# Optimization experiments

Hardware: AMD Instinct MI355X
Metric: run time of the kernel (lower is better)

Reference implementation:

```python
import jax, jax.numpy as jnp
import numpy as np

BITS = 4
MAXQ = 15          # (1 << BITS) - 1
PACK = 32 // BITS  # 8 values packed per int32


def dequantize(qweight, qzeros, scales, g_idx):
    """GPTQ 4-bit dequant. qweight: [K//8, N] int32, qzeros: [G, N//8] int32,
    scales: [G, N] float, g_idx: [K] int32 -> dense W [K, N] float."""
    N = qweight.shape[1]
    shifts = (jnp.arange(PACK, dtype=jnp.uint32) * BITS)  # [8]
    qw = qweight.astype(jnp.uint32)
    # unpack along K: k = row*8 + j  (matches shifter = (k % 8) * bits)
    w_int = ((qw[:, None, :] >> shifts[None, :, None]) & MAXQ).reshape(-1, N)  # [K, N]
    qz = qzeros.astype(jnp.uint32)
    # unpack along N: n = col*8 + j  (matches zeros_shifter = (n % 8) * bits)
    z_int = ((qz[:, :, None] >> shifts[None, None, :]) & MAXQ).reshape(qzeros.shape[0], -1) + 1  # [G, N]
    dt = scales.dtype
    # group-wise dequant: w = (q - zero) * scale, gathered per-row via g_idx
    return (w_int.astype(dt) - z_int[g_idx].astype(dt)) * scales[g_idx]


def setup_inputs() -> dict:
    key = jax.random.key(0)
    k1, k2, k3, k4, k5 = jax.random.split(key, 5)
    M, K, N, GS = 128, 4096, 11008, 128
    G = K // GS
    x = jax.random.normal(k1, (M, K), dtype=jnp.float32)
    qweight = jax.random.randint(k2, (K // PACK, N), 0, 2147483647, dtype=jnp.int32)
    qzeros = jax.random.randint(k3, (G, N // PACK), 0, 2147483647, dtype=jnp.int32)
    scales = jax.random.uniform(k4, (G, N), dtype=jnp.float32, minval=0.001, maxval=0.01)
    bias = jax.random.normal(k5, (N,), dtype=jnp.float32)
    g_idx = (jnp.arange(K, dtype=jnp.int32) // GS).astype(jnp.int32)
    return {"x": x, "qweight": qweight, "qzeros": qzeros, "scales": scales,
            "bias": bias, "g_idx": g_idx}


def reference(x, qweight, qzeros, scales, bias, g_idx):
    w = dequantize(qweight, qzeros, scales, g_idx)  # [K, N]
    return x @ w + bias
```

## Files before the change

### kernel.cpp

```cpp
#include <hip/hip_runtime.h>
#include <stdint.h>


#define M_DIM 128
#define K_DIM 4096
#define N_DIM 11008
#define GS    128
#define SPLIT 4
#define STEPS 32
#define PART_STRIDE ((size_t)M_DIM * N_DIM)

typedef _Float16 half8  __attribute__((ext_vector_type(8)));
typedef _Float16 half4t __attribute__((ext_vector_type(4)));
typedef _Float16 half2t __attribute__((ext_vector_type(2)));
typedef float    f32x4  __attribute__((ext_vector_type(4)));

__global__ void k_prep(const float* __restrict__ x, const int* __restrict__ qzeros,
                       const float* __restrict__ scales,
                       _Float16* __restrict__ xf, half2t* __restrict__ zsc) {
    int b = blockIdx.x, t = threadIdx.x;
    if (b < 256) {
        int slot = b * 256 + t;
        int lane = slot & 63;
        int pair = slot >> 6;
        int mt = pair >> 7, kb = pair & 127;
        int row = mt * 16 + (lane & 15);
        int col = kb * 32 + (lane >> 4) * 8;
        const float* px = x + (size_t)row * K_DIM + col;
        float4 v0 = *(const float4*)px;
        float4 v1 = *(const float4*)(px + 4);
        half8 o;
        o[0] = (_Float16)v0.x; o[1] = (_Float16)v0.y;
        o[2] = (_Float16)v0.z; o[3] = (_Float16)v0.w;
        o[4] = (_Float16)v1.x; o[5] = (_Float16)v1.y;
        o[6] = (_Float16)v1.z; o[7] = (_Float16)v1.w;
        *(half8*)(xf + (size_t)slot * 8) = o;
    } else {
        b -= 256;
        int g = b / 43;
        int n = (b - g * 43) * 256 + t;
        unsigned qz = (unsigned)qzeros[g * (N_DIM / 8) + (n >> 3)];
        float z1 = (float)((qz >> ((n & 7) * 4)) & 15u) + 1.0f;
        float s  = scales[g * N_DIM + n];
        half2t o;
        o[0] = (_Float16)s;
        o[1] = (_Float16)(-z1 * s);
        zsc[g * N_DIM + n] = o;
    }
}

__device__ __forceinline__ half8 dequant8(unsigned q, half2t S2, half2t Z2) {
    const half2t BIAS = __builtin_bit_cast(half2t, 0x64006400u);
    half2t w[4];
#pragma unroll
    for (int p = 0; p < 4; ++p) {
        unsigned r = __builtin_amdgcn_perm(q, q, 0x00010001u * (unsigned)p);
        unsigned t = (r & 0x00F0000Fu) | 0x64006400u;
        w[p] = __builtin_elementwise_fma(__builtin_bit_cast(half2t, t) - BIAS, S2, Z2);
    }
    half4t w01 = __builtin_shufflevector(w[0], w[1], 0, 1, 2, 3);
    half4t w23 = __builtin_shufflevector(w[2], w[3], 0, 1, 2, 3);
    return __builtin_shufflevector(w01, w23, 0, 1, 2, 3, 4, 5, 6, 7);
}

__global__ __launch_bounds__(256, 4)
void k_gemm(const _Float16* __restrict__ xf,
            const int*      __restrict__ qweight,
            const half2t*   __restrict__ zsc,
            float*          __restrict__ part)
{
    const int tid  = threadIdx.x;
    const int lane = tid & 63;
    const int w    = tid >> 6;
    const int q    = lane >> 4;
    const int lr   = lane & 15;

    const int n0 = blockIdx.x * 64;
    const int by = blockIdx.y;

    int ncol[4];
#pragma unroll
    for (int j = 0; j < 4; ++j) ncol[j] = n0 + j * 16 + lr;

    f32x4 acc[2][4];
#pragma unroll
    for (int f = 0; f < 2; ++f)
#pragma unroll
        for (int j = 0; j < 4; ++j)
            acc[f][j] = (f32x4){0.f, 0.f, 0.f, 0.f};

    const _Float16* pa0 = xf + (((size_t)(2 * w) * 128 + by * 32) << 9) + lane * 8;
    const _Float16* pa1 = pa0 + ((size_t)128 << 9);
    const int* pq = qweight + (size_t)(by * 128 + q) * N_DIM;
    const half2t* pz = zsc + (size_t)(by * 8) * N_DIM;

    half8 a0 = *(const half8*)pa0;
    half8 a1 = *(const half8*)pa1;
    unsigned qc[4];
    half2t   zc[4];
#pragma unroll
    for (int j = 0; j < 4; ++j) {
        qc[j] = (unsigned)pq[ncol[j]];
        zc[j] = pz[ncol[j]];
    }

    for (int g = 0; g < 8; ++g) {
        const half2t SC = { (_Float16)1.0f, (_Float16)0.0625f };
        half2t S2[4], Z2[4];
#pragma unroll
        for (int j = 0; j < 4; ++j) {
            half2t ss = __builtin_shufflevector(zc[j], zc[j], 0, 0);
            S2[j] = ss * SC;
            Z2[j] = __builtin_shufflevector(zc[j], zc[j], 1, 1);
        }

#pragma unroll
        for (int t = 0; t < 4; ++t) {
            const int s  = g * 4 + t;
            const int sn = (s + 1 < STEPS) ? s + 1 : s;

            half8 na0 = *(const half8*)(pa0 + (size_t)sn * 512);
            half8 na1 = *(const half8*)(pa1 + (size_t)sn * 512);
            unsigned nq[4];
#pragma unroll
            for (int j = 0; j < 4; ++j)
                nq[j] = (unsigned)pq[(size_t)sn * 4 * N_DIM + ncol[j]];
            half2t nz[4];
            if (t == 3) {
                int gn = (g + 1 < 8) ? g + 1 : g;
#pragma unroll
                for (int j = 0; j < 4; ++j)
                    nz[j] = pz[(size_t)gn * N_DIM + ncol[j]];
            }

#pragma unroll
            for (int j = 0; j < 4; ++j) {
                half8 bf = dequant8(qc[j], S2[j], Z2[j]);
                acc[0][j] = __builtin_amdgcn_mfma_f32_16x16x32_f16(a0, bf, acc[0][j], 0, 0, 0);
                acc[1][j] = __builtin_amdgcn_mfma_f32_16x16x32_f16(a1, bf, acc[1][j], 0, 0, 0);
            }

            a0 = na0; a1 = na1;
#pragma unroll
            for (int j = 0; j < 4; ++j) qc[j] = nq[j];
            if (t == 3) {
#pragma unroll
                for (int j = 0; j < 4; ++j) zc[j] = nz[j];
            }
        }
    }

    float* po = part + (size_t)by * PART_STRIDE;
#pragma unroll
    for (int f = 0; f < 2; ++f) {
        int mrow = w * 32 + f * 16 + q * 4;
#pragma unroll
        for (int j = 0; j < 4; ++j)
#pragma unroll
            for (int r = 0; r < 4; ++r)
                po[(size_t)(mrow + r) * N_DIM + ncol[j]] = acc[f][j][r];
    }
}

__global__ void k_reduce(const float* __restrict__ part, const float* __restrict__ bias,
                         float* __restrict__ out) {
    int i = (blockIdx.x * 256 + threadIdx.x) * 4;
    int m = i / N_DIM;
    int n = i - m * N_DIM;
    f32x4 s = *(const f32x4*)(bias + n);
#pragma unroll
    for (int sp = 0; sp < SPLIT; ++sp)
        s += *(const f32x4*)(part + sp * PART_STRIDE + i);
    *(f32x4*)(out + i) = s;
}

extern "C" void kernel_launch(void* const* d_in, const int* in_sizes, int n_in,
                              void* d_out, int out_size, void* d_ws, size_t ws_size,
                              hipStream_t stream) {
    const float* x       = (const float*)d_in[0];
    const int*   qweight = (const int*)d_in[1];
    const int*   qzeros  = (const int*)d_in[2];
    const float* scales  = (const float*)d_in[3];
    const float* bias    = (const float*)d_in[4];

    char* ws = (char*)d_ws;
    _Float16* xf   = (_Float16*)ws;
    half2t*   zsc  = (half2t*)(ws + 1048576);
    float*    part = (float*)(ws + 1048576 + 1409024);

    k_prep  <<<dim3(1632),            dim3(256), 0, stream>>>(x, qzeros, scales, xf, zsc);
    k_gemm  <<<dim3(N_DIM/64, SPLIT), dim3(256), 0, stream>>>(xf, qweight, zsc, part);
    k_reduce<<<dim3(1376),            dim3(256), 0, stream>>>(part, bias, (float*)d_out);
}
```

Measured before the change: 110.3 us.

## Remove split-K and reduce kernel; write output with bias directly from GEMM

Drops the 4-way split-K and its partial-sum buffer and reduce kernel. Each of the 172 blocks now runs all 128 K-steps and adds the bias in its epilogue. It also deepens the register prefetch of activations and weights to two steps ahead. This avoids writing and re-reading four fp32 partial outputs (about 22 MB) and one launch, but cuts the grid to 172 blocks on a 256-CU device, so parallelism drops and fewer loads are in flight.

```diff
diff --git a/kernel.cpp b/kernel.cpp
--- a/kernel.cpp
+++ b/kernel.cpp
@@ -6,9 +6,7 @@
 #define K_DIM 4096
 #define N_DIM 11008
 #define GS    128
-#define SPLIT 4
-#define STEPS 32
-#define PART_STRIDE ((size_t)M_DIM * N_DIM)
+#define STEPS 128
 
 typedef _Float16 half8  __attribute__((ext_vector_type(8)));
 typedef _Float16 half4t __attribute__((ext_vector_type(4)));
@@ -67,7 +65,8 @@
 void k_gemm(const _Float16* __restrict__ xf,
             const int*      __restrict__ qweight,
             const half2t*   __restrict__ zsc,
-            float*          __restrict__ part)
+            const float*    __restrict__ bias,
+            float*          __restrict__ out)
 {
     const int tid  = threadIdx.x;
     const int lane = tid & 63;
@@ -76,7 +75,6 @@
     const int lr   = lane & 15;
 
     const int n0 = blockIdx.x * 64;
-    const int by = blockIdx.y;
 
     int ncol[4];
 #pragma unroll
@@ -89,22 +87,29 @@
         for (int j = 0; j < 4; ++j)
             acc[f][j] = (f32x4){0.f, 0.f, 0.f, 0.f};
 
-    const _Float16* pa0 = xf + (((size_t)(2 * w) * 128 + by * 32) << 9) + lane * 8;
+    const _Float16* pa0 = xf + (((size_t)(2 * w) * 128) << 9) + lane * 8;
     const _Float16* pa1 = pa0 + ((size_t)128 << 9);
-    const int* pq = qweight + (size_t)(by * 128 + q) * N_DIM;
-    const half2t* pz = zsc + (size_t)(by * 8) * N_DIM;
+    const int*      pq  = qweight + (size_t)q * N_DIM;
+    const half2t*   pz  = zsc;
 
-    half8 a0 = *(const half8*)pa0;
-    half8 a1 = *(const half8*)pa1;
-    unsigned qc[4];
+    half8    A0[2], A1[2];
+    unsigned Q[2][4];
     half2t   zc[4];
 #pragma unroll
-    for (int j = 0; j < 4; ++j) {
-        qc[j] = (unsigned)pq[ncol[j]];
-        zc[j] = pz[ncol[j]];
+    for (int c = 0; c < 2; ++c) {
+        A0[c] = *(const half8*)(pa0 + (size_t)c * 512);
+        A1[c] = *(const half8*)(pa1 + (size_t)c * 512);
+#pragma unroll
+        for (int j = 0; j < 4; ++j)
+            Q[c][j] = (unsigned)pq[(size_t)c * 4 * N_DIM + ncol[j]];
     }
+#pragma unroll
+    for (int j = 0; j < 4; ++j) zc[j] = pz[ncol[j]];
+    float bv[4];
+#pragma unroll
+    for (int j = 0; j < 4; ++j) bv[j] = bias[ncol[j]];
 
-    for (int g = 0; g < 8; ++g) {
+    for (int g = 0; g < 32; ++g) {
         const half2t SC = { (_Float16)1.0f, (_Float16)0.0625f };
         half2t S2[4], Z2[4];
 #pragma unroll
@@ -117,17 +122,18 @@
 #pragma unroll
         for (int t = 0; t < 4; ++t) {
             const int s  = g * 4 + t;
-            const int sn = (s + 1 < STEPS) ? s + 1 : s;
+            const int c  = s & 1;
+            const int sn = (s + 2 < STEPS) ? s + 2 : STEPS - 1;
 
-            half8 na0 = *(const half8*)(pa0 + (size_t)sn * 512);
-            half8 na1 = *(const half8*)(pa1 + (size_t)sn * 512);
-            unsigned nq[4];
+            half8 ta0 = *(const half8*)(pa0 + (size_t)sn * 512);
+            half8 ta1 = *(const half8*)(pa1 + (size_t)sn * 512);
+            unsigned tq[4];
 #pragma unroll
             for (int j = 0; j < 4; ++j)
-                nq[j] = (unsigned)pq[(size_t)sn * 4 * N_DIM + ncol[j]];
+                tq[j] = (unsigned)pq[(size_t)sn * 4 * N_DIM + ncol[j]];
             half2t nz[4];
             if (t == 3) {
-                int gn = (g + 1 < 8) ? g + 1 : g;
+                int gn = (g + 1 < 32) ? g + 1 : g;
 #pragma unroll
                 for (int j = 0; j < 4; ++j)
                     nz[j] = pz[(size_t)gn * N_DIM + ncol[j]];
@@ -135,14 +141,14 @@
 
 #pragma unroll
             for (int j = 0; j < 4; ++j) {
-                half8 bf = dequant8(qc[j], S2[j], Z2[j]);
-                acc[0][j] = __builtin_amdgcn_mfma_f32_16x16x32_f16(a0, bf, acc[0][j], 0, 0, 0);
-                acc[1][j] = __builtin_amdgcn_mfma_f32_16x16x32_f16(a1, bf, acc[1][j], 0, 0, 0);
+                half8 bf = dequant8(Q[c][j], S2[j], Z2[j]);
+                acc[0][j] = __builtin_amdgcn_mfma_f32_16x16x32_f16(A0[c], bf, acc[0][j], 0, 0, 0);
+                acc[1][j] = __builtin_amdgcn_mfma_f32_16x16x32_f16(A1[c], bf, acc[1][j], 0, 0, 0);
             }
 
-            a0 = na0; a1 = na1;
+            A0[c] = ta0; A1[c] = ta1;
 #pragma unroll
-            for (int j = 0; j < 4; ++j) qc[j] = nq[j];
+            for (int j = 0; j < 4; ++j) Q[c][j] = tq[j];
             if (t == 3) {
 #pragma unroll
                 for (int j = 0; j < 4; ++j) zc[j] = nz[j];
@@ -150,7 +156,6 @@
         }
     }
 
-    float* po = part + (size_t)by * PART_STRIDE;
 #pragma unroll
     for (int f = 0; f < 2; ++f) {
         int mrow = w * 32 + f * 16 + q * 4;
@@ -158,20 +163,8 @@
         for (int j = 0; j < 4; ++j)
 #pragma unroll
             for (int r = 0; r < 4; ++r)
-                po[(size_t)(mrow + r) * N_DIM + ncol[j]] = acc[f][j][r];
+                out[(size_t)(mrow + r) * N_DIM + ncol[j]] = acc[f][j][r] + bv[j];
     }
-}
-
-__global__ void k_reduce(const float* __restrict__ part, const float* __restrict__ bias,
-                         float* __restrict__ out) {
-    int i = (blockIdx.x * 256 + threadIdx.x) * 4;
-    int m = i / N_DIM;
-    int n = i - m * N_DIM;
-    f32x4 s = *(const f32x4*)(bias + n);
-#pragma unroll
-    for (int sp = 0; sp < SPLIT; ++sp)
-        s += *(const f32x4*)(part + sp * PART_STRIDE + i);
-    *(f32x4*)(out + i) = s;
 }
 
 extern "C" void kernel_launch(void* const* d_in, const int* in_sizes, int n_in,
@@ -184,11 +177,9 @@
     const float* bias    = (const float*)d_in[4];
 
     char* ws = (char*)d_ws;
-    _Float16* xf   = (_Float16*)ws;
-    half2t*   zsc  = (half2t*)(ws + 1048576);
-    float*    part = (float*)(ws + 1048576 + 1409024);
+    _Float16* xf  = (_Float16*)ws;
+    half2t*   zsc = (half2t*)(ws + 1048576);
 
-    k_prep  <<<dim3(1632),            dim3(256), 0, stream>>>(x, qzeros, scales, xf, zsc);
-    k_gemm  <<<dim3(N_DIM/64, SPLIT), dim3(256), 0, stream>>>(xf, qweight, zsc, part);
-    k_reduce<<<dim3(1376),            dim3(256), 0, stream>>>(part, bias, (float*)d_out);
+    k_prep<<<dim3(1632),      dim3(256), 0, stream>>>(x, qzeros, scales, xf, zsc);
+    k_gemm<<<dim3(N_DIM/64),  dim3(256), 0, stream>>>(xf, qweight, zsc, bias, (float*)d_out);
 }
```

Result: slower. 117.7 us (+6.8%).
